# Kernel tuning notes

Measured on AMD Instinct MI355X. Metric: run time of the kernel, lower is better.

Reference implementation:

```python
import jax, jax.numpy as jnp
import numpy as np
from jax import lax

B = 16384
D_MODEL = 84
N_EXPERTS = 2
TOP_K = 2
HIDDEN = 2048


def _conv(x, w, b):
    # x: [N,C,H,W], w: [O,I,kh,kw] (torch OIHW), VALID padding, stride 1
    y = lax.conv_general_dilated(x, w, (1, 1), 'VALID',
                                 dimension_numbers=('NCHW', 'OIHW', 'NCHW'))
    return y + b[None, :, None, None]


def _maxpool2(x):
    return lax.reduce_window(x, -jnp.inf, lax.max,
                             (1, 1, 2, 2), (1, 1, 2, 2), 'VALID')


def setup_inputs() -> dict:
    key = jax.random.key(0)
    ks = jax.random.split(key, 17)
    s = 0.05
    return {
        'x': jax.random.normal(ks[0], (B, 3, 32, 32), jnp.float32),
        'conv1_w': jax.random.normal(ks[1], (6, 3, 5, 5), jnp.float32) * s,
        'conv1_b': jax.random.normal(ks[2], (6,), jnp.float32) * s,
        'conv2_w': jax.random.normal(ks[3], (16, 6, 5, 5), jnp.float32) * s,
        'conv2_b': jax.random.normal(ks[4], (16,), jnp.float32) * s,
        'fc1_w': jax.random.normal(ks[5], (400, 120), jnp.float32) * s,
        'fc1_b': jax.random.normal(ks[6], (120,), jnp.float32) * s,
        'fc2_w': jax.random.normal(ks[7], (120, 84), jnp.float32) * s,
        'fc2_b': jax.random.normal(ks[8], (84,), jnp.float32) * s,
        'gate_w': jax.random.normal(ks[9], (D_MODEL, N_EXPERTS), jnp.float32) * s,
        'exp_w1': jax.random.normal(ks[10], (N_EXPERTS, D_MODEL, HIDDEN), jnp.float32) * s,
        'exp_b1': jax.random.normal(ks[11], (N_EXPERTS, HIDDEN), jnp.float32) * s,
        'exp_w2': jax.random.normal(ks[12], (N_EXPERTS, HIDDEN, D_MODEL), jnp.float32) * s,
        'exp_b2': jax.random.normal(ks[13], (N_EXPERTS, D_MODEL), jnp.float32) * s,
        'fc3_w': jax.random.normal(ks[14], (84, 10), jnp.float32) * s,
        'fc3_b': jax.random.normal(ks[15], (10,), jnp.float32) * s,
    }


def _moe(x, gate_w, exp_w1, exp_b1, exp_w2, exp_b2):
    # tutel top-k gate: softmax over expert logits, select top-k, renormalize
    n = x.shape[0]
    scores = jax.nn.softmax(x @ gate_w, axis=-1)          # [N,E]
    top_v, top_i = lax.top_k(scores, TOP_K)               # [N,k]
    gates = top_v / jnp.sum(top_v, axis=-1, keepdims=True)
    # dense combine weights [N,E] (zero where not routed)
    comb = jnp.zeros((n, N_EXPERTS), x.dtype).at[
        jnp.arange(n)[:, None], top_i].set(gates)
    # grouped expert FFN (E=2: evaluate both, weight-combine)
    h = jax.nn.relu(jnp.einsum('nd,edh->enh', x, exp_w1) + exp_b1[:, None, :])
    y = jnp.einsum('enh,ehd->end', h, exp_w2) + exp_b2[:, None, :]  # [E,N,D]
    return jnp.einsum('ne,end->nd', comb, y)


def reference(x, conv1_w, conv1_b, conv2_w, conv2_b, fc1_w, fc1_b,
              fc2_w, fc2_b, gate_w, exp_w1, exp_b1, exp_w2, exp_b2,
              fc3_w, fc3_b):
    h = _maxpool2(jax.nn.relu(_conv(x, conv1_w, conv1_b)))   # [B,6,14,14]
    h = _maxpool2(jax.nn.relu(_conv(h, conv2_w, conv2_b)))   # [B,16,5,5]
    h = h.reshape(-1, 16 * 5 * 5)                            # [B,400]
    h = jax.nn.relu(h @ fc1_w + fc1_b)                       # [B,120]
    h = jax.nn.relu(h @ fc2_w + fc2_b)                       # [B,84]
    h = _moe(h, gate_w, exp_w1, exp_b1, exp_w2, exp_b2)      # [B,84]
    return h @ fc3_w + fc3_b                                 # [B,10]
```

## Files before the change

kernel.cpp:

```cpp
#include <hip/hip_runtime.h>
#include <stdint.h>

typedef unsigned short u16;
typedef __attribute__((ext_vector_type(8))) short s8v;
typedef __attribute__((ext_vector_type(4))) float f4v;
typedef __fp16 h2v __attribute__((ext_vector_type(2)));

__device__ __forceinline__ float bu2f(u16 u) {
  return __uint_as_float(((uint32_t)u) << 16);
}
__device__ __forceinline__ u16 f2bu(float f) {
  uint32_t u = __float_as_uint(f);
  u += 0x7fffu + ((u >> 16) & 1u);
  return (u16)(u >> 16);
}

union U32H2 { uint32_t u; h2v h; };

__device__ __forceinline__ uint32_t pk2h(float a, float b) {
  U32H2 x;
  x.h = __builtin_amdgcn_cvt_pkrtz(a, b);
  return x.u;
}

#if __has_builtin(__builtin_amdgcn_fdot2)
__device__ __forceinline__ float fdot2u(uint32_t a, uint32_t b, float c) {
  U32H2 ua, ub;
  ua.u = a; ub.u = b;
  return __builtin_amdgcn_fdot2(ua.h, ub.h, c, false);
}
#else
__device__ __forceinline__ float fdot2u(uint32_t a, uint32_t b, float c) {
  U32H2 ua, ub;
  ua.u = a; ub.u = b;
  c = fmaf((float)ua.h.x, (float)ub.h.x, c);
  return fmaf((float)ua.h.y, (float)ub.h.y, c);
}
#endif

template <bool F32> struct In;
template <> struct In<true> {
  static __device__ __forceinline__ float ld(const void* p, long i) {
    return ((const float*)p)[i];
  }
};
template <> struct In<false> {
  static __device__ __forceinline__ float ld(const void* p, long i) {
    return bu2f(((const u16*)p)[i]);
  }
};

__global__ void k_detect(const u16* __restrict__ x, int* __restrict__ flag) {
  __shared__ int s[64];
  int cnt = 0;
  for (int i = threadIdx.x; i < 2048; i += 64) {
    int e = (x[i] >> 7) & 0xFF;
    cnt += (e >= 96 && e <= 134) ? 1 : 0;
  }
  s[threadIdx.x] = cnt;
  __syncthreads();
  if (threadIdx.x == 0) {
    int t = 0;
    for (int i = 0; i < 64; ++i) t += s[i];
    *flag = (t >= 1843) ? 0 : 1;
  }
}

__device__ __forceinline__ u16 f2h16(float f) {
  __fp16 h = (__fp16)f;
  u16 r;
  __builtin_memcpy(&r, &h, 2);
  return r;
}

template <bool INF32>
__global__ __launch_bounds__(256) void k_trans(
    const int* __restrict__ flag,
    const void* __restrict__ fc1w, const void* __restrict__ fc2w,
    const void* __restrict__ ew1, const void* __restrict__ ew2,
    const void* __restrict__ c1w, const void* __restrict__ c1b,
    const void* __restrict__ c2w, const void* __restrict__ c2b,
    u16* __restrict__ fc1t, u16* __restrict__ fc2t,
    u16* __restrict__ w1t, u16* __restrict__ w2t,
    uint32_t* __restrict__ cdw) {
  if (*flag != (INF32 ? 1 : 0)) return;
  long gid = (long)blockIdx.x * 256 + threadIdx.x;
  if (gid < 53248) {
    int n = (int)(gid / 416), k = (int)(gid % 416);
    fc1t[gid] = (n < 120 && k < 400) ? f2bu(In<INF32>::ld(fc1w, (long)k * 120 + n)) : (u16)0;
  } else if (gid < 65536) {
    long i = gid - 53248;
    int n = (int)(i / 128), k = (int)(i % 128);
    fc2t[i] = (n < 84 && k < 120) ? f2bu(In<INF32>::ld(fc2w, (long)k * 84 + n)) : (u16)0;
  } else if (gid < 458752) {
    long i = gid - 65536;
    int e = (int)(i / 196608);
    long r = i % 196608;
    int n = (int)(r / 96), k = (int)(r % 96);
    w1t[i] = (k < 84) ? f2bu(In<INF32>::ld(ew1, ((long)e * 84 + k) * 2048 + n)) : (u16)0;
  } else if (gid < 851968) {
    long i = gid - 458752;
    int e = (int)(i / 196608);
    long r = i % 196608;
    int n = (int)(r / 2048), k = (int)(r % 2048);
    w2t[i] = (n < 84) ? f2bu(In<INF32>::ld(ew2, ((long)e * 2048 + k) * 84 + n)) : (u16)0;
  } else if (gid < 853700) {
    long i = gid - 851968;
    if (i < 270) {
      int p = (int)(i % 3), ky = (int)((i / 3) % 5);
      int ic = (int)((i / 15) % 3), c = (int)(i / 45);
      long base = (((long)c * 3 + ic) * 5 + ky) * 5;
      float w0 = In<INF32>::ld(c1w, base + 2 * p);
      float w1 = (2 * p + 1 < 5) ? In<INF32>::ld(c1w, base + 2 * p + 1) : 0.f;
      cdw[i] = (uint32_t)f2h16(w0) | ((uint32_t)f2h16(w1) << 16);
    } else if (i < 1710) {
      long j = i - 270;
      int p = (int)(j % 3), ky = (int)((j / 3) % 5);
      int ic = (int)((j / 15) % 6), c = (int)(j / 90);
      long base = (((long)c * 6 + ic) * 5 + ky) * 5;
      float w0 = In<INF32>::ld(c2w, base + 2 * p);
      float w1 = (2 * p + 1 < 5) ? In<INF32>::ld(c2w, base + 2 * p + 1) : 0.f;
      cdw[270 + j] = (uint32_t)f2h16(w0) | ((uint32_t)f2h16(w1) << 16);
    } else if (i < 1716) {
      ((float*)(cdw + 1710))[i - 1710] = In<INF32>::ld(c1b, i - 1710);
    } else if (i < 1732) {
      ((float*)(cdw + 1716))[i - 1716] = In<INF32>::ld(c2b, i - 1716);
    }
  }
}

#define CIMG 5
template <bool INF32>
__global__ __launch_bounds__(256) void k_conv(
    const int* __restrict__ flag,
    const void* __restrict__ x,
    const uint32_t* __restrict__ cdw,
    u16* __restrict__ p2, int Btot) {
  if (*flag != (INF32 ? 1 : 0)) return;
  __shared__ u16 sxh[CIMG * 3 * 32 * 36];
  __shared__ u16 sp1h[CIMG * 6 * 14 * 18];
  const uint32_t* cd1 = cdw;
  const uint32_t* cd2 = cdw + 270;
  const float* cb1 = (const float*)(cdw + 1710);
  const float* cb2 = (const float*)(cdw + 1716);
  const int tid = threadIdx.x;
  const long gimg0 = (long)blockIdx.x * CIMG;

  for (int r = tid; r < CIMG * 96; r += 256) {
    *(uint32_t*)(sxh + (size_t)r * 36 + 32) = 0;
    *(uint32_t*)(sxh + (size_t)r * 36 + 34) = 0;
  }
  for (int r = tid; r < CIMG * 84; r += 256) {
    *(uint32_t*)(sp1h + (size_t)r * 18 + 14) = 0;
    *(uint32_t*)(sp1h + (size_t)r * 18 + 16) = 0;
  }

  for (int i = tid; i < CIMG * 96; i += 256) {
    int img = i / 96, rem = i - img * 96;
    if (gimg0 + img < Btot) {
      long goff = (gimg0 + img) * 3072 + (long)rem * 32;
      u16* dst = sxh + (size_t)i * 36;
      if (!INF32) {
        const uint32_t* src = (const uint32_t*)((const u16*)x + goff);
#pragma unroll
        for (int j = 0; j < 16; ++j) {
          uint32_t d = src[j];
          *(uint32_t*)(dst + 2 * j) =
              pk2h(__uint_as_float(d << 16), __uint_as_float(d & 0xffff0000u));
        }
      } else {
        const float* src = (const float*)x + goff;
#pragma unroll
        for (int j = 0; j < 16; ++j)
          *(uint32_t*)(dst + 2 * j) = pk2h(src[2 * j], src[2 * j + 1]);
      }
    }
  }
  __syncthreads();

  for (int task = tid; task < CIMG * 196; task += 256) {
    int img = task / 196, pos = task - img * 196;
    if (gimg0 + img >= Btot) continue;
    int py = pos / 14, px = pos - py * 14;
    int x0 = 2 * px, y0 = 2 * py;
    float acc[6][4];
#pragma unroll
    for (int c = 0; c < 6; ++c) {
      float bv = cb1[c];
      acc[c][0] = bv; acc[c][1] = bv; acc[c][2] = bv; acc[c][3] = bv;
    }
    for (int ic = 0; ic < 3; ++ic) {
      uint32_t A[6][4], S[6][3];
      const u16* rb = sxh + ((size_t)(img * 3 + ic) * 32 + y0) * 36 + x0;
#pragma unroll
      for (int r = 0; r < 6; ++r) {
#pragma unroll
        for (int p = 0; p < 4; ++p)
          A[r][p] = *(const uint32_t*)(rb + (size_t)r * 36 + 2 * p);
#pragma unroll
        for (int p = 0; p < 3; ++p)
          S[r][p] = (A[r][p] >> 16) | (A[r][p + 1] << 16);
      }
#pragma unroll
      for (int c = 0; c < 6; ++c) {
        const uint32_t* wb = cd1 + ((c * 3 + ic) * 5) * 3;
#pragma unroll
        for (int ky = 0; ky < 5; ++ky) {
#pragma unroll
          for (int p = 0; p < 3; ++p) {
            uint32_t w = wb[ky * 3 + p];
            acc[c][0] = fdot2u(A[ky][p], w, acc[c][0]);
            acc[c][1] = fdot2u(S[ky][p], w, acc[c][1]);
            acc[c][2] = fdot2u(A[ky + 1][p], w, acc[c][2]);
            acc[c][3] = fdot2u(S[ky + 1][p], w, acc[c][3]);
          }
        }
      }
    }
#pragma unroll
    for (int c = 0; c < 6; ++c) {
      float m = fmaxf(0.f, fmaxf(fmaxf(acc[c][0], acc[c][1]),
                                 fmaxf(acc[c][2], acc[c][3])));
      sp1h[((size_t)(img * 6 + c) * 14 + py) * 18 + px] = f2h16(m);
    }
  }
  __syncthreads();

  for (int task = tid; task < CIMG * 100; task += 256) {
    int img = task / 100, r0 = task - img * 100;
    if (gimg0 + img >= Btot) continue;
    int grp = r0 / 25, pos = r0 - grp * 25;
    int py = pos / 5, px = pos - py * 5;
    int x0 = 2 * px, y0 = 2 * py;
    int c0 = grp * 4;
    float acc[4][4];
#pragma unroll
    for (int c = 0; c < 4; ++c) {
      float bv = cb2[c0 + c];
      acc[c][0] = bv; acc[c][1] = bv; acc[c][2] = bv; acc[c][3] = bv;
    }
    for (int ic = 0; ic < 6; ++ic) {
      uint32_t A[6][4], S[6][3];
      const u16* rb = sp1h + ((size_t)(img * 6 + ic) * 14 + y0) * 18 + x0;
#pragma unroll
      for (int r = 0; r < 6; ++r) {
#pragma unroll
        for (int p = 0; p < 4; ++p)
          A[r][p] = *(const uint32_t*)(rb + (size_t)r * 18 + 2 * p);
#pragma unroll
        for (int p = 0; p < 3; ++p)
          S[r][p] = (A[r][p] >> 16) | (A[r][p + 1] << 16);
      }
#pragma unroll
      for (int c = 0; c < 4; ++c) {
        const uint32_t* wb = cd2 + (((c0 + c) * 6 + ic) * 5) * 3;
#pragma unroll
        for (int ky = 0; ky < 5; ++ky) {
#pragma unroll
          for (int p = 0; p < 3; ++p) {
            uint32_t w = wb[ky * 3 + p];
            acc[c][0] = fdot2u(A[ky][p], w, acc[c][0]);
            acc[c][1] = fdot2u(S[ky][p], w, acc[c][1]);
            acc[c][2] = fdot2u(A[ky + 1][p], w, acc[c][2]);
            acc[c][3] = fdot2u(S[ky + 1][p], w, acc[c][3]);
          }
        }
      }
    }
    u16* pout = p2 + (gimg0 + img) * 416;
#pragma unroll
    for (int c = 0; c < 4; ++c) {
      float m = fmaxf(0.f, fmaxf(fmaxf(acc[c][0], acc[c][1]),
                                 fmaxf(acc[c][2], acc[c][3])));
      pout[(c0 + c) * 25 + py * 5 + px] = f2bu(m);
    }
  }

  for (int i = tid; i < CIMG * 16; i += 256) {
    int img = i / 16;
    if (gimg0 + img < Btot) p2[(gimg0 + img) * 416 + 400 + (i & 15)] = 0;
  }
}

template <bool INF32>
__global__ __launch_bounds__(256) void k_fcA(
    const int* __restrict__ flag,
    const u16* __restrict__ p2,
    const u16* __restrict__ fc1t, const u16* __restrict__ fc2t,
    const void* __restrict__ fc1b, const void* __restrict__ fc2b,
    const void* __restrict__ gw,
    u16* __restrict__ a2buf, float* __restrict__ scbuf) {
  if (*flag != (INF32 ? 1 : 0)) return;
  __shared__ __align__(16) char smem[62976];
  u16* a2s = (u16*)smem;
  u16* hs = (u16*)(smem + 13312);
  u16* wbuf = (u16*)(smem + 31232);
  u16* xs = (u16*)(smem + 57856);

  const int tid = threadIdx.x;
  const int wv = tid >> 6, ln = tid & 63;
  const int m = ln & 15, quad = ln >> 4;
  const long t0 = (long)blockIdx.x * 64;
  const int row0 = wv * 16 + quad * 4;

  for (int i = tid; i < 30720 / 4; i += 256) ((uint32_t*)smem)[i] = 0;

  f4v acc1[8];
#pragma unroll
  for (int i = 0; i < 8; ++i) acc1[i] = (f4v){0.f, 0.f, 0.f, 0.f};
  for (int s = 0; s < 13; ++s) {
    {
      int r = tid >> 2, c0 = (tid & 3) * 8;
      *(uint4*)(xs + r * 40 + c0) =
          *(const uint4*)(p2 + (t0 + r) * 416 + s * 32 + c0);
      int n = tid >> 1, cw = (tid & 1) * 16;
      *(uint4*)(wbuf + n * 40 + cw) = *(const uint4*)(fc1t + (long)n * 416 + s * 32 + cw);
      *(uint4*)(wbuf + n * 40 + cw + 8) =
          *(const uint4*)(fc1t + (long)n * 416 + s * 32 + cw + 8);
    }
    __syncthreads();
    s8v a = *(const s8v*)(xs + (wv * 16 + m) * 40 + quad * 8);
#pragma unroll
    for (int nt = 0; nt < 8; ++nt) {
      s8v b = *(const s8v*)(wbuf + (nt * 16 + m) * 40 + quad * 8);
      acc1[nt] = __builtin_amdgcn_mfma_f32_16x16x32_bf16(a, b, acc1[nt], 0, 0, 0);
    }
    __syncthreads();
  }
#pragma unroll
  for (int nt = 0; nt < 8; ++nt) {
    int n = nt * 16 + m;
    if (n < 120) {
      float bv = In<INF32>::ld(fc1b, n);
#pragma unroll
      for (int r = 0; r < 4; ++r)
        hs[(row0 + r) * 136 + n] = f2bu(fmaxf(acc1[nt][r] + bv, 0.f));
    }
  }
  __syncthreads();

  for (int i = tid; i < 1536; i += 256) {
    int n = i >> 4, c0 = (i & 15) * 8;
    *(uint4*)(wbuf + n * 136 + c0) = *(const uint4*)(fc2t + n * 128 + c0);
  }
  __syncthreads();
  f4v acc2[6];
#pragma unroll
  for (int i = 0; i < 6; ++i) acc2[i] = (f4v){0.f, 0.f, 0.f, 0.f};
  for (int s = 0; s < 4; ++s) {
    s8v a = *(const s8v*)(hs + (wv * 16 + m) * 136 + s * 32 + quad * 8);
#pragma unroll
    for (int nt = 0; nt < 6; ++nt) {
      s8v b = *(const s8v*)(wbuf + (nt * 16 + m) * 136 + s * 32 + quad * 8);
      acc2[nt] = __builtin_amdgcn_mfma_f32_16x16x32_bf16(a, b, acc2[nt], 0, 0, 0);
    }
  }
  __syncthreads();
#pragma unroll
  for (int nt = 0; nt < 6; ++nt) {
    int n = nt * 16 + m;
    if (n < 84) {
      float bv = In<INF32>::ld(fc2b, n);
#pragma unroll
      for (int r = 0; r < 4; ++r)
        a2s[(row0 + r) * 104 + n] = f2bu(fmaxf(acc2[nt][r] + bv, 0.f));
    }
  }
  __syncthreads();

  if (tid < 64) {
    const u16* xr = a2s + tid * 104;
    float l0 = 0.f, l1 = 0.f;
    for (int k = 0; k < 84; ++k) {
      float xv = bu2f(xr[k]);
      l0 = fmaf(xv, In<INF32>::ld(gw, 2 * k), l0);
      l1 = fmaf(xv, In<INF32>::ld(gw, 2 * k + 1), l1);
    }
    float mx = fmaxf(l0, l1);
    float e0 = __expf(l0 - mx), e1 = __expf(l1 - mx);
    float inv = 1.f / (e0 + e1);
    *(float2*)(scbuf + (t0 + tid) * 2) = make_float2(e0 * inv, e1 * inv);
  }
  for (int i = tid; i < 832; i += 256) {
    int r = i / 13, c0 = (i - r * 13) * 8;
    *(uint4*)(a2buf + (t0 + r) * 104 + c0) = *(const uint4*)(a2s + r * 104 + c0);
  }
}

template <bool INF32>
__global__ __launch_bounds__(256) void k_exp(
    const int* __restrict__ flag,
    const u16* __restrict__ a2buf, const float* __restrict__ scbuf,
    const u16* __restrict__ w1t, const u16* __restrict__ w2t,
    const void* __restrict__ eb1, const void* __restrict__ eb2,
    float* __restrict__ ybuf, int Btok) {
  if (*flag != (INF32 ? 1 : 0)) return;
  __shared__ __align__(16) char smem[57856];
  u16* a2s = (u16*)smem;
  u16* hs = (u16*)(smem + 13312);
  u16* wbuf = (u16*)(smem + 30720);
  float* scs = (float*)(smem + 57344);

  const int tid = threadIdx.x;
  const int wv = tid >> 6, ln = tid & 63;
  const int m = ln & 15, quad = ln >> 4;
  const int e = blockIdx.y;
  const long t0 = (long)blockIdx.x * 64;
  const int row0 = wv * 16 + quad * 4;
  const u16* w1te = w1t + (long)e * 196608;
  const u16* w2te = w2t + (long)e * 196608;

  for (int i = tid; i < 832; i += 256) {
    int r = i / 13, c0 = (i - r * 13) * 8;
    *(uint4*)(a2s + r * 104 + c0) = *(const uint4*)(a2buf + (t0 + r) * 104 + c0);
  }
  if (tid < 64) scs[tid] = scbuf[(t0 + tid) * 2 + e];
  __syncthreads();

  f4v acce[6];
#pragma unroll
  for (int i = 0; i < 6; ++i) acce[i] = (f4v){0.f, 0.f, 0.f, 0.f};
  for (int c = 0; c < 16; ++c) {
    const int n0 = c * 128;
    if (c) __syncthreads();
    for (int i = tid; i < 1536; i += 256) {
      int nl = i / 12, c0 = (i - nl * 12) * 8;
      *(uint4*)(wbuf + nl * 104 + c0) =
          *(const uint4*)(w1te + (long)(n0 + nl) * 96 + c0);
    }
    __syncthreads();
    f4v acch[8];
#pragma unroll
    for (int i = 0; i < 8; ++i) acch[i] = (f4v){0.f, 0.f, 0.f, 0.f};
    for (int s = 0; s < 3; ++s) {
      s8v a = *(const s8v*)(a2s + (wv * 16 + m) * 104 + s * 32 + quad * 8);
#pragma unroll
      for (int nt = 0; nt < 8; ++nt) {
        s8v b = *(const s8v*)(wbuf + (nt * 16 + m) * 104 + s * 32 + quad * 8);
        acch[nt] = __builtin_amdgcn_mfma_f32_16x16x32_bf16(a, b, acch[nt], 0, 0, 0);
      }
    }
#pragma unroll
    for (int nt = 0; nt < 8; ++nt) {
      float bv = In<INF32>::ld(eb1, (long)e * 2048 + n0 + nt * 16 + m);
#pragma unroll
      for (int r = 0; r < 4; ++r)
        hs[(row0 + r) * 136 + nt * 16 + m] = f2bu(fmaxf(acch[nt][r] + bv, 0.f));
    }
    __syncthreads();
    for (int i = tid; i < 1536; i += 256) {
      int n = i >> 4, c0 = (i & 15) * 8;
      *(uint4*)(wbuf + n * 136 + c0) =
          *(const uint4*)(w2te + (long)n * 2048 + n0 + c0);
    }
    __syncthreads();
    for (int s = 0; s < 4; ++s) {
      s8v a = *(const s8v*)(hs + (wv * 16 + m) * 136 + s * 32 + quad * 8);
#pragma unroll
      for (int nt = 0; nt < 6; ++nt) {
        s8v b = *(const s8v*)(wbuf + (nt * 16 + m) * 136 + s * 32 + quad * 8);
        acce[nt] = __builtin_amdgcn_mfma_f32_16x16x32_bf16(a, b, acce[nt], 0, 0, 0);
      }
    }
  }

#pragma unroll
  for (int nt = 0; nt < 6; ++nt) {
    int d = nt * 16 + m;
    float bv = (d < 84) ? In<INF32>::ld(eb2, (long)e * 84 + d) : 0.f;
#pragma unroll
    for (int r = 0; r < 4; ++r) {
      float sc = scs[row0 + r];
      ybuf[((size_t)e * Btok + t0 + row0 + r) * 96 + d] = sc * (acce[nt][r] + bv);
    }
  }
}

template <bool INF32>
__global__ __launch_bounds__(256) void k_fc3(
    const int* __restrict__ flag,
    const float* __restrict__ ybuf,
    const void* __restrict__ w3, const void* __restrict__ b3,
    void* __restrict__ out, int Btok) {
  if (*flag != (INF32 ? 1 : 0)) return;
  __shared__ float sw3[840];
  __shared__ float sb3[10];
  const int tid = threadIdx.x;
  const long t0 = (long)blockIdx.x * 64;
  for (int i = tid; i < 840; i += 256) sw3[i] = In<INF32>::ld(w3, i);
  if (tid < 10) sb3[tid] = In<INF32>::ld(b3, tid);
  __syncthreads();
  for (int idx = tid; idx < 640; idx += 256) {
    int tk = idx / 10, cc = idx - tk * 10;
    const float* y0r = ybuf + (t0 + tk) * 96;
    const float* y1r = ybuf + ((size_t)Btok + t0 + tk) * 96;
    float acc = sb3[cc];
    for (int d = 0; d < 84; ++d)
      acc = fmaf(y0r[d] + y1r[d], sw3[d * 10 + cc], acc);
    long oi = (t0 + tk) * 10 + cc;
    if (INF32) ((float*)out)[oi] = acc;
    else ((u16*)out)[oi] = f2bu(acc);
  }
}

extern "C" void kernel_launch(void* const* d_in, const int* in_sizes, int n_in,
                              void* d_out, int out_size, void* d_ws, size_t ws_size,
                              hipStream_t stream) {
  const int B = in_sizes[0] / 3072;
  char* wsb = (char*)d_ws;
  int* flag = (int*)wsb;
  u16* p2 = (u16*)(wsb + 64);
  u16* fc1t = p2 + (size_t)B * 416;
  u16* fc2t = fc1t + 53248;
  u16* w1t = fc2t + 12288;
  u16* w2t = w1t + 393216;
  uint32_t* cdw = (uint32_t*)(w2t + 393216);
  u16* a2buf = (u16*)(cdw + 1732);
  float* scbuf = (float*)(a2buf + (size_t)B * 104);
  float* ybuf = scbuf + (size_t)B * 2;

  k_detect<<<1, 64, 0, stream>>>((const u16*)d_in[0], flag);

  k_trans<false><<<3336, 256, 0, stream>>>(flag, d_in[5], d_in[7], d_in[10],
                                           d_in[12], d_in[1], d_in[2], d_in[3],
                                           d_in[4], fc1t, fc2t, w1t, w2t, cdw);
  k_trans<true><<<3336, 256, 0, stream>>>(flag, d_in[5], d_in[7], d_in[10],
                                          d_in[12], d_in[1], d_in[2], d_in[3],
                                          d_in[4], fc1t, fc2t, w1t, w2t, cdw);

  const int convGrid = (B + CIMG - 1) / CIMG;
  k_conv<false><<<convGrid, 256, 0, stream>>>(flag, d_in[0], cdw, p2, B);
  k_conv<true><<<convGrid, 256, 0, stream>>>(flag, d_in[0], cdw, p2, B);

  k_fcA<false><<<B / 64, 256, 0, stream>>>(flag, p2, fc1t, fc2t, d_in[6],
                                           d_in[8], d_in[9], a2buf, scbuf);
  k_fcA<true><<<B / 64, 256, 0, stream>>>(flag, p2, fc1t, fc2t, d_in[6],
                                          d_in[8], d_in[9], a2buf, scbuf);

  dim3 eg(B / 64, 2);
  k_exp<false><<<eg, 256, 0, stream>>>(flag, a2buf, scbuf, w1t, w2t, d_in[11],
                                       d_in[13], ybuf, B);
  k_exp<true><<<eg, 256, 0, stream>>>(flag, a2buf, scbuf, w1t, w2t, d_in[11],
                                      d_in[13], ybuf, B);

  k_fc3<false><<<B / 64, 256, 0, stream>>>(flag, ybuf, d_in[14], d_in[15],
                                           d_out, B);
  k_fc3<true><<<B / 64, 256, 0, stream>>>(flag, ybuf, d_in[14], d_in[15],
                                          d_out, B);
}
```

Baseline: 593.0 us.

## Fold weight transposes into conv kernel and drop dual-dtype kernel launches

Replaces the templated pairs of kernels, one instantiation per input dtype, with single kernels that branch at runtime on the detected mode. This halves the launch count. The separate detect and conv-weight prep kernels merge into one small init kernel. The large weight transpose moves into the tail of the conv kernel, spread across its blocks, so it no longer needs its own launch. Other changes: the smem row pitch widens from 36 to 38, and launch_bounds occupancy hints are added. The trade-off is runtime-mode branches inside hot loops and extra register pressure in the conv kernel.

```diff
diff --git a/kernel.cpp b/kernel.cpp
--- a/kernel.cpp
+++ b/kernel.cpp
@@ -13,6 +13,15 @@
   uint32_t u = __float_as_uint(f);
   u += 0x7fffu + ((u >> 16) & 1u);
   return (u16)(u >> 16);
+}
+__device__ __forceinline__ u16 f2h16(float f) {
+  __fp16 h = (__fp16)f;
+  u16 r;
+  __builtin_memcpy(&r, &h, 2);
+  return r;
+}
+__device__ __forceinline__ float ldin(int m, const void* p, long i) {
+  return m ? ((const float*)p)[i] : bu2f(((const u16*)p)[i]);
 }
 
 union U32H2 { uint32_t u; h2v h; };
@@ -38,107 +47,67 @@
 }
 #endif
 
-template <bool F32> struct In;
-template <> struct In<true> {
-  static __device__ __forceinline__ float ld(const void* p, long i) {
-    return ((const float*)p)[i];
-  }
-};
-template <> struct In<false> {
-  static __device__ __forceinline__ float ld(const void* p, long i) {
-    return bu2f(((const u16*)p)[i]);
-  }
-};
-
-__global__ void k_detect(const u16* __restrict__ x, int* __restrict__ flag) {
-  __shared__ int s[64];
+__global__ __launch_bounds__(256) void k_init(
+    const u16* __restrict__ x,
+    const void* __restrict__ c1w, const void* __restrict__ c1b,
+    const void* __restrict__ c2w, const void* __restrict__ c2b,
+    int* __restrict__ flag, uint32_t* __restrict__ cdw) {
+  __shared__ int s[256];
+  __shared__ int smode;
+  const int tid = threadIdx.x;
   int cnt = 0;
-  for (int i = threadIdx.x; i < 2048; i += 64) {
+  for (int i = tid; i < 2048; i += 256) {
     int e = (x[i] >> 7) & 0xFF;
     cnt += (e >= 96 && e <= 134) ? 1 : 0;
   }
-  s[threadIdx.x] = cnt;
-  __syncthreads();
-  if (threadIdx.x == 0) {
+  s[tid] = cnt;
+  __syncthreads();
+  if (tid == 0) {
     int t = 0;
-    for (int i = 0; i < 64; ++i) t += s[i];
-    *flag = (t >= 1843) ? 0 : 1;
-  }
-}
-
-__device__ __forceinline__ u16 f2h16(float f) {
-  __fp16 h = (__fp16)f;
-  u16 r;
-  __builtin_memcpy(&r, &h, 2);
-  return r;
-}
-
-template <bool INF32>
-__global__ __launch_bounds__(256) void k_trans(
-    const int* __restrict__ flag,
-    const void* __restrict__ fc1w, const void* __restrict__ fc2w,
-    const void* __restrict__ ew1, const void* __restrict__ ew2,
-    const void* __restrict__ c1w, const void* __restrict__ c1b,
-    const void* __restrict__ c2w, const void* __restrict__ c2b,
-    u16* __restrict__ fc1t, u16* __restrict__ fc2t,
-    u16* __restrict__ w1t, u16* __restrict__ w2t,
-    uint32_t* __restrict__ cdw) {
-  if (*flag != (INF32 ? 1 : 0)) return;
-  long gid = (long)blockIdx.x * 256 + threadIdx.x;
-  if (gid < 53248) {
-    int n = (int)(gid / 416), k = (int)(gid % 416);
-    fc1t[gid] = (n < 120 && k < 400) ? f2bu(In<INF32>::ld(fc1w, (long)k * 120 + n)) : (u16)0;
-  } else if (gid < 65536) {
-    long i = gid - 53248;
-    int n = (int)(i / 128), k = (int)(i % 128);
-    fc2t[i] = (n < 84 && k < 120) ? f2bu(In<INF32>::ld(fc2w, (long)k * 84 + n)) : (u16)0;
-  } else if (gid < 458752) {
-    long i = gid - 65536;
-    int e = (int)(i / 196608);
-    long r = i % 196608;
-    int n = (int)(r / 96), k = (int)(r % 96);
-    w1t[i] = (k < 84) ? f2bu(In<INF32>::ld(ew1, ((long)e * 84 + k) * 2048 + n)) : (u16)0;
-  } else if (gid < 851968) {
-    long i = gid - 458752;
-    int e = (int)(i / 196608);
-    long r = i % 196608;
-    int n = (int)(r / 2048), k = (int)(r % 2048);
-    w2t[i] = (n < 84) ? f2bu(In<INF32>::ld(ew2, ((long)e * 2048 + k) * 84 + n)) : (u16)0;
-  } else if (gid < 853700) {
-    long i = gid - 851968;
+    for (int i = 0; i < 256; ++i) t += s[i];
+    int m = (t >= 1843) ? 0 : 1;
+    *flag = m;
+    smode = m;
+  }
+  __syncthreads();
+  const int mode = smode;
+  for (int i = tid; i < 1732; i += 256) {
     if (i < 270) {
-      int p = (int)(i % 3), ky = (int)((i / 3) % 5);
-      int ic = (int)((i / 15) % 3), c = (int)(i / 45);
-      long base = (((long)c * 3 + ic) * 5 + ky) * 5;
-      float w0 = In<INF32>::ld(c1w, base + 2 * p);
-      float w1 = (2 * p + 1 < 5) ? In<INF32>::ld(c1w, base + 2 * p + 1) : 0.f;
+      int p = i % 3, ky = (i / 3) % 5, ic = (i / 15) % 3, c = i / 45;
+      long b = (((long)c * 3 + ic) * 5 + ky) * 5;
+      float w0 = ldin(mode, c1w, b + 2 * p);
+      float w1 = (2 * p + 1 < 5) ? ldin(mode, c1w, b + 2 * p + 1) : 0.f;
       cdw[i] = (uint32_t)f2h16(w0) | ((uint32_t)f2h16(w1) << 16);
     } else if (i < 1710) {
-      long j = i - 270;
-      int p = (int)(j % 3), ky = (int)((j / 3) % 5);
-      int ic = (int)((j / 15) % 6), c = (int)(j / 90);
-      long base = (((long)c * 6 + ic) * 5 + ky) * 5;
-      float w0 = In<INF32>::ld(c2w, base + 2 * p);
-      float w1 = (2 * p + 1 < 5) ? In<INF32>::ld(c2w, base + 2 * p + 1) : 0.f;
-      cdw[270 + j] = (uint32_t)f2h16(w0) | ((uint32_t)f2h16(w1) << 16);
+      int j = i - 270;
+      int p = j % 3, ky = (j / 3) % 5, ic = (j / 15) % 6, c = j / 90;
+      long b = (((long)c * 6 + ic) * 5 + ky) * 5;
+      float w0 = ldin(mode, c2w, b + 2 * p);
+      float w1 = (2 * p + 1 < 5) ? ldin(mode, c2w, b + 2 * p + 1) : 0.f;
+      cdw[i] = (uint32_t)f2h16(w0) | ((uint32_t)f2h16(w1) << 16);
     } else if (i < 1716) {
-      ((float*)(cdw + 1710))[i - 1710] = In<INF32>::ld(c1b, i - 1710);
-    } else if (i < 1732) {
-      ((float*)(cdw + 1716))[i - 1716] = In<INF32>::ld(c2b, i - 1716);
+      ((float*)(cdw + 1710))[i - 1710] = ldin(mode, c1b, i - 1710);
+    } else {
+      ((float*)(cdw + 1716))[i - 1716] = ldin(mode, c2b, i - 1716);
     }
   }
 }
 
 #define CIMG 5
-template <bool INF32>
-__global__ __launch_bounds__(256) void k_conv(
+#define SXW 38
+__global__ __launch_bounds__(256, 3) void k_conv(
     const int* __restrict__ flag,
     const void* __restrict__ x,
     const uint32_t* __restrict__ cdw,
-    u16* __restrict__ p2, int Btot) {
-  if (*flag != (INF32 ? 1 : 0)) return;
-  __shared__ u16 sxh[CIMG * 3 * 32 * 36];
+    const void* __restrict__ fc1w, const void* __restrict__ fc2w,
+    const void* __restrict__ ew1, const void* __restrict__ ew2,
+    u16* __restrict__ p2,
+    u16* __restrict__ fc1t, u16* __restrict__ fc2t,
+    u16* __restrict__ w1t, u16* __restrict__ w2t,
+    int Btot) {
+  __shared__ u16 sxh[CIMG * 3 * 32 * SXW];
   __shared__ u16 sp1h[CIMG * 6 * 14 * 18];
+  const int mode = *flag;
   const uint32_t* cd1 = cdw;
   const uint32_t* cd2 = cdw + 270;
   const float* cb1 = (const float*)(cdw + 1710);
@@ -147,8 +116,9 @@
   const long gimg0 = (long)blockIdx.x * CIMG;
 
   for (int r = tid; r < CIMG * 96; r += 256) {
-    *(uint32_t*)(sxh + (size_t)r * 36 + 32) = 0;
-    *(uint32_t*)(sxh + (size_t)r * 36 + 34) = 0;
+    *(uint32_t*)(sxh + (size_t)r * SXW + 32) = 0;
+    *(uint32_t*)(sxh + (size_t)r * SXW + 34) = 0;
+    *(uint32_t*)(sxh + (size_t)r * SXW + 36) = 0;
   }
   for (int r = tid; r < CIMG * 84; r += 256) {
     *(uint32_t*)(sp1h + (size_t)r * 18 + 14) = 0;
@@ -159,8 +129,8 @@
     int img = i / 96, rem = i - img * 96;
     if (gimg0 + img < Btot) {
       long goff = (gimg0 + img) * 3072 + (long)rem * 32;
-      u16* dst = sxh + (size_t)i * 36;
-      if (!INF32) {
+      u16* dst = sxh + (size_t)i * SXW;
+      if (!mode) {
         const uint32_t* src = (const uint32_t*)((const u16*)x + goff);
 #pragma unroll
         for (int j = 0; j < 16; ++j) {
@@ -191,12 +161,12 @@
     }
     for (int ic = 0; ic < 3; ++ic) {
       uint32_t A[6][4], S[6][3];
-      const u16* rb = sxh + ((size_t)(img * 3 + ic) * 32 + y0) * 36 + x0;
+      const u16* rb = sxh + ((size_t)(img * 3 + ic) * 32 + y0) * SXW + x0;
 #pragma unroll
       for (int r = 0; r < 6; ++r) {
 #pragma unroll
         for (int p = 0; p < 4; ++p)
-          A[r][p] = *(const uint32_t*)(rb + (size_t)r * 36 + 2 * p);
+          A[r][p] = *(const uint32_t*)(rb + (size_t)r * SXW + 2 * p);
 #pragma unroll
         for (int p = 0; p < 3; ++p)
           S[r][p] = (A[r][p] >> 16) | (A[r][p + 1] << 16);
@@ -280,23 +250,54 @@
     int img = i / 16;
     if (gimg0 + img < Btot) p2[(gimg0 + img) * 416 + 400 + (i & 15)] = 0;
   }
-}
-
-template <bool INF32>
-__global__ __launch_bounds__(256) void k_fcA(
+
+  {
+    long base = (long)blockIdx.x * 260;
+    long end = base + 260;
+    if (end > 851968) end = 851968;
+    for (long gid = base + tid; gid < end; gid += 256) {
+      if (gid < 53248) {
+        int n = (int)(gid / 416), k = (int)(gid % 416);
+        fc1t[gid] = (n < 120 && k < 400)
+                        ? f2bu(ldin(mode, fc1w, (long)k * 120 + n)) : (u16)0;
+      } else if (gid < 65536) {
+        long i = gid - 53248;
+        int n = (int)(i / 128), k = (int)(i % 128);
+        fc2t[i] = (n < 84 && k < 120)
+                      ? f2bu(ldin(mode, fc2w, (long)k * 84 + n)) : (u16)0;
+      } else if (gid < 458752) {
+        long i = gid - 65536;
+        int e = (int)(i / 196608);
+        long r = i % 196608;
+        int n = (int)(r / 96), k = (int)(r % 96);
+        w1t[i] = (k < 84)
+                     ? f2bu(ldin(mode, ew1, ((long)e * 84 + k) * 2048 + n)) : (u16)0;
+      } else {
+        long i = gid - 458752;
+        int e = (int)(i / 196608);
+        long r = i % 196608;
+        int n = (int)(r / 2048), k = (int)(r % 2048);
+        w2t[i] = (n < 84)
+                     ? f2bu(ldin(mode, ew2, ((long)e * 2048 + k) * 84 + n)) : (u16)0;
+      }
+    }
+  }
+}
+
+__global__ __launch_bounds__(256, 2) void k_fcA(
     const int* __restrict__ flag,
     const u16* __restrict__ p2,
     const u16* __restrict__ fc1t, const u16* __restrict__ fc2t,
     const void* __restrict__ fc1b, const void* __restrict__ fc2b,
     const void* __restrict__ gw,
     u16* __restrict__ a2buf, float* __restrict__ scbuf) {
-  if (*flag != (INF32 ? 1 : 0)) return;
   __shared__ __align__(16) char smem[62976];
   u16* a2s = (u16*)smem;
   u16* hs = (u16*)(smem + 13312);
   u16* wbuf = (u16*)(smem + 31232);
   u16* xs = (u16*)(smem + 57856);
 
+  const int mode = *flag;
   const int tid = threadIdx.x;
   const int wv = tid >> 6, ln = tid & 63;
   const int m = ln & 15, quad = ln >> 4;
@@ -331,7 +332,7 @@
   for (int nt = 0; nt < 8; ++nt) {
     int n = nt * 16 + m;
     if (n < 120) {
-      float bv = In<INF32>::ld(fc1b, n);
+      float bv = ldin(mode, fc1b, n);
 #pragma unroll
       for (int r = 0; r < 4; ++r)
         hs[(row0 + r) * 136 + n] = f2bu(fmaxf(acc1[nt][r] + bv, 0.f));
@@ -360,7 +361,7 @@
   for (int nt = 0; nt < 6; ++nt) {
     int n = nt * 16 + m;
     if (n < 84) {
-      float bv = In<INF32>::ld(fc2b, n);
+      float bv = ldin(mode, fc2b, n);
 #pragma unroll
       for (int r = 0; r < 4; ++r)
         a2s[(row0 + r) * 104 + n] = f2bu(fmaxf(acc2[nt][r] + bv, 0.f));
@@ -373,8 +374,8 @@
     float l0 = 0.f, l1 = 0.f;
     for (int k = 0; k < 84; ++k) {
       float xv = bu2f(xr[k]);
-      l0 = fmaf(xv, In<INF32>::ld(gw, 2 * k), l0);
-      l1 = fmaf(xv, In<INF32>::ld(gw, 2 * k + 1), l1);
+      l0 = fmaf(xv, ldin(mode, gw, 2 * k), l0);
+      l1 = fmaf(xv, ldin(mode, gw, 2 * k + 1), l1);
     }
     float mx = fmaxf(l0, l1);
     float e0 = __expf(l0 - mx), e1 = __expf(l1 - mx);
@@ -387,20 +388,19 @@
   }
 }
 
-template <bool INF32>
-__global__ __launch_bounds__(256) void k_exp(
+__global__ __launch_bounds__(256, 2) void k_exp(
     const int* __restrict__ flag,
     const u16* __restrict__ a2buf, const float* __restrict__ scbuf,
     const u16* __restrict__ w1t, const u16* __restrict__ w2t,
     const void* __restrict__ eb1, const void* __restrict__ eb2,
     float* __restrict__ ybuf, int Btok) {
-  if (*flag != (INF32 ? 1 : 0)) return;
   __shared__ __align__(16) char smem[57856];
   u16* a2s = (u16*)smem;
   u16* hs = (u16*)(smem + 13312);
   u16* wbuf = (u16*)(smem + 30720);
   float* scs = (float*)(smem + 57344);
 
+  const int mode = *flag;
   const int tid = threadIdx.x;
   const int wv = tid >> 6, ln = tid & 63;
   const int m = ln & 15, quad = ln >> 4;
@@ -442,7 +442,7 @@
     }
 #pragma unroll
     for (int nt = 0; nt < 8; ++nt) {
-      float bv = In<INF32>::ld(eb1, (long)e * 2048 + n0 + nt * 16 + m);
+      float bv = ldin(mode, eb1, (long)e * 2048 + n0 + nt * 16 + m);
 #pragma unroll
       for (int r = 0; r < 4; ++r)
         hs[(row0 + r) * 136 + nt * 16 + m] = f2bu(fmaxf(acch[nt][r] + bv, 0.f));
@@ -467,7 +467,7 @@
 #pragma unroll
   for (int nt = 0; nt < 6; ++nt) {
     int d = nt * 16 + m;
-    float bv = (d < 84) ? In<INF32>::ld(eb2, (long)e * 84 + d) : 0.f;
+    float bv = (d < 84) ? ldin(mode, eb2, (long)e * 84 + d) : 0.f;
 #pragma unroll
     for (int r = 0; r < 4; ++r) {
       float sc = scs[row0 + r];
@@ -476,19 +476,18 @@
   }
 }
 
-template <bool INF32>
 __global__ __launch_bounds__(256) void k_fc3(
     const int* __restrict__ flag,
     const float* __restrict__ ybuf,
     const void* __restrict__ w3, const void* __restrict__ b3,
     void* __restrict__ out, int Btok) {
-  if (*flag != (INF32 ? 1 : 0)) return;
   __shared__ float sw3[840];
   __shared__ float sb3[10];
+  const int mode = *flag;
   const int tid = threadIdx.x;
   const long t0 = (long)blockIdx.x * 64;
-  for (int i = tid; i < 840; i += 256) sw3[i] = In<INF32>::ld(w3, i);
-  if (tid < 10) sb3[tid] = In<INF32>::ld(b3, tid);
+  for (int i = tid; i < 840; i += 256) sw3[i] = ldin(mode, w3, i);
+  if (tid < 10) sb3[tid] = ldin(mode, b3, tid);
   __syncthreads();
   for (int idx = tid; idx < 640; idx += 256) {
     int tk = idx / 10, cc = idx - tk * 10;
@@ -498,7 +497,7 @@
     for (int d = 0; d < 84; ++d)
       acc = fmaf(y0r[d] + y1r[d], sw3[d * 10 + cc], acc);
     long oi = (t0 + tk) * 10 + cc;
-    if (INF32) ((float*)out)[oi] = acc;
+    if (mode) ((float*)out)[oi] = acc;
     else ((u16*)out)[oi] = f2bu(acc);
   }
 }
@@ -519,32 +518,20 @@
   float* scbuf = (float*)(a2buf + (size_t)B * 104);
   float* ybuf = scbuf + (size_t)B * 2;
 
-  k_detect<<<1, 64, 0, stream>>>((const u16*)d_in[0], flag);
-
-  k_trans<false><<<3336, 256, 0, stream>>>(flag, d_in[5], d_in[7], d_in[10],
-                                           d_in[12], d_in[1], d_in[2], d_in[3],
-                                           d_in[4], fc1t, fc2t, w1t, w2t, cdw);
-  k_trans<true><<<3336, 256, 0, stream>>>(flag, d_in[5], d_in[7], d_in[10],
-                                          d_in[12], d_in[1], d_in[2], d_in[3],
-                                          d_in[4], fc1t, fc2t, w1t, w2t, cdw);
+  k_init<<<1, 256, 0, stream>>>((const u16*)d_in[0], d_in[1], d_in[2],
+                                d_in[3], d_in[4], flag, cdw);
 
   const int convGrid = (B + CIMG - 1) / CIMG;
-  k_conv<false><<<convGrid, 256, 0, stream>>>(flag, d_in[0], cdw, p2, B);
-  k_conv<true><<<convGrid, 256, 0, stream>>>(flag, d_in[0], cdw, p2, B);
-
-  k_fcA<false><<<B / 64, 256, 0, stream>>>(flag, p2, fc1t, fc2t, d_in[6],
-                                           d_in[8], d_in[9], a2buf, scbuf);
-  k_fcA<true><<<B / 64, 256, 0, stream>>>(flag, p2, fc1t, fc2t, d_in[6],
-                                          d_in[8], d_in[9], a2buf, scbuf);
+  k_conv<<<convGrid, 256, 0, stream>>>(flag, d_in[0], cdw, d_in[5], d_in[7],
+                                       d_in[10], d_in[12], p2, fc1t, fc2t,
+                                       w1t, w2t, B);
+
+  k_fcA<<<B / 64, 256, 0, stream>>>(flag, p2, fc1t, fc2t, d_in[6], d_in[8],
+                                    d_in[9], a2buf, scbuf);
 
   dim3 eg(B / 64, 2);
-  k_exp<false><<<eg, 256, 0, stream>>>(flag, a2buf, scbuf, w1t, w2t, d_in[11],
-                                       d_in[13], ybuf, B);
-  k_exp<true><<<eg, 256, 0, stream>>>(flag, a2buf, scbuf, w1t, w2t, d_in[11],
-                                      d_in[13], ybuf, B);
-
-  k_fc3<false><<<B / 64, 256, 0, stream>>>(flag, ybuf, d_in[14], d_in[15],
-                                           d_out, B);
-  k_fc3<true><<<B / 64, 256, 0, stream>>>(flag, ybuf, d_in[14], d_in[15],
-                                          d_out, B);
-}
+  k_exp<<<eg, 256, 0, stream>>>(flag, a2buf, scbuf, w1t, w2t, d_in[11],
+                                d_in[13], ybuf, B);
+
+  k_fc3<<<B / 64, 256, 0, stream>>>(flag, ybuf, d_in[14], d_in[15], d_out, B);
+}
```

New measurement: 619.0 us. +4.4%, slower.
